# Kernel tuning notes

Hardware: AMD Instinct MI355X
Metric: run time of the kernel (lower is better)

Reference implementation:

```python
import jax, jax.numpy as jnp
import numpy as np

N = 100000   # num nodes
E = 1000000  # num edges
IN, H, OUT = 128, 64, 64
THR = 0.1      # lcs_threshold
LN_EPS = 1e-5


def setup_inputs() -> dict:
    key = jax.random.key(0)
    ks = jax.random.split(key, 8)
    x = jax.random.normal(ks[0], (N, IN), dtype=jnp.float32)
    edge_index = jax.random.randint(ks[1], (2, E), 0, N, dtype=jnp.int32)
    W1 = jax.random.normal(ks[2], (IN, H), dtype=jnp.float32) / np.float32(np.sqrt(IN))
    b1 = jnp.zeros((H,), jnp.float32)
    W2 = jax.random.normal(ks[3], (H, OUT), dtype=jnp.float32) / np.float32(np.sqrt(H))
    b2 = jnp.zeros((OUT,), jnp.float32)
    ln_gamma = jnp.ones((H,), jnp.float32)
    ln_beta = jnp.zeros((H,), jnp.float32)
    return {"x": x, "W1": W1, "b1": b1, "W2": W2, "b2": b2,
            "ln_gamma": ln_gamma, "ln_beta": ln_beta, "edge_index": edge_index}


def _gcn_conv(h_in, W, b, src, dst, ew, n):
    """PyG GCNConv: D^-1/2 (A+I) D^-1/2 (h_in @ W) + b, with edge weights ew.
    Masked edges (ew=0) contribute neither messages nor degree -> equivalent to
    filtering them out."""
    h = h_in @ W                                   # [n, d_out]
    deg = jax.ops.segment_sum(ew, dst, num_segments=n) + 1.0  # +1 self-loop
    dis = jax.lax.rsqrt(deg)                       # deg >= 1, finite
    norm = dis[src] * dis[dst] * ew                # [E]
    agg = jax.ops.segment_sum(h[src] * norm[:, None], dst, num_segments=n)
    agg = agg + h * (dis * dis)[:, None]           # self-loop term
    return agg + b


def _layer_norm(h, gamma, beta):
    mu = jnp.mean(h, axis=-1, keepdims=True)
    var = jnp.mean(jnp.square(h - mu), axis=-1, keepdims=True)
    return (h - mu) * jax.lax.rsqrt(var + LN_EPS) * gamma + beta


def reference(x, W1, b1, W2, b2, ln_gamma, ln_beta, edge_index):
    src, dst = edge_index[0], edge_index[1]
    n = x.shape[0]
    ones_e = jnp.ones((src.shape[0],), x.dtype)

    # layer 0: no LCS filtering (i == 0)
    h = _gcn_conv(x, W1, b1, src, dst, ones_e, n)
    h = _layer_norm(h, ln_gamma, ln_beta)
    h = jax.nn.relu(h)  # dropout: inference mode (identity)

    # layer 1: LCS filtering via node scores = min-max normalized L2 norm
    s = jnp.linalg.norm(h, axis=1)
    s = (s - s.min()) / (s.max() - s.min() + 1e-8)
    mask = (s[dst] > THR).astype(x.dtype)

    out = _gcn_conv(h, W2, b2, src, dst, mask, n)
    return jax.nn.log_softmax(out, axis=1)
```

## Files before the change

### kernel.cpp

```cpp
#include <hip/hip_runtime.h>
#include <math.h>

#define N_NODES 100000
#define N_EDGES 1000000
#define IN_F 128
#define H_F 64
#define THRV 0.1f
#define LN_EPS 1e-5f
#define GRID_AGG 2048

#define BSHIFT 9
#define NB 196
#define BCAP 6144
#define EPB 2048
#define NPB ((N_EDGES + EPB - 1) / EPB)

static __device__ __forceinline__ float wave_sum(float x) {
  for (int o = 32; o > 0; o >>= 1) x += __shfl_xor(x, o, 64);
  return x;
}
static __device__ __forceinline__ float wave_max(float x) {
  for (int o = 32; o > 0; o >>= 1) x = fmaxf(x, __shfl_xor(x, o, 64));
  return x;
}
static __device__ __forceinline__ unsigned short f2bf(float f) {
  unsigned u = __float_as_uint(f);
  u = (u + 0x7FFFu + ((u >> 16) & 1u)) >> 16;
  return (unsigned short)u;
}
static __device__ __forceinline__ float bf2f(unsigned short b) {
  return __uint_as_float(((unsigned)b) << 16);
}


__global__ __launch_bounds__(256) void k_part(const int* __restrict__ src,
                                              const int* __restrict__ dst,
                                              int* __restrict__ bcnt,
                                              int* __restrict__ part) {
  __shared__ int h[NB];
  __shared__ int cur[NB];
  int t = threadIdx.x;
  for (int i = t; i < NB; i += 256) h[i] = 0;
  __syncthreads();
  int base = blockIdx.x * EPB;
  int d[8];
#pragma unroll
  for (int i = 0; i < 8; ++i) {
    int e = base + t + i * 256;
    d[i] = (e < N_EDGES) ? dst[e] : -1;
  }
#pragma unroll
  for (int i = 0; i < 8; ++i)
    if (d[i] >= 0) atomicAdd(&h[d[i] >> BSHIFT], 1);
  __syncthreads();
  for (int i = t; i < NB; i += 256) {
    int c = h[i];
    cur[i] = c ? atomicAdd(&bcnt[i], c) : 0;
  }
  __syncthreads();
#pragma unroll
  for (int i = 0; i < 8; ++i) {
    if (d[i] >= 0) {
      int e = base + t + i * 256;
      int b = d[i] >> BSHIFT;
      int pos = atomicAdd(&cur[b], 1);
      part[b * BCAP + pos] = src[e] | ((d[i] & 511) << 17);
    }
  }
}

__global__ __launch_bounds__(256) void k_build(
    const int* __restrict__ part, const int* __restrict__ bcnt,
    int* __restrict__ indeg, int* __restrict__ offs, float* __restrict__ dis1,
    int* __restrict__ csr_src) {
  __shared__ int cnt[512];
  __shared__ int slds[256];
  int b = blockIdx.x;
  int t = threadIdx.x;
  int beg = b * BCAP;
  int end = beg + bcnt[b];
  for (int i = t; i < 512; i += 256) cnt[i] = 0;
  __syncthreads();
  for (int i = beg + t; i < end; i += 256)
    atomicAdd(&cnt[(part[i] >> 17) & 511], 1);
  __syncthreads();
  int a0 = cnt[2 * t], a1 = cnt[2 * t + 1];
  int pairsum = a0 + a1;
  slds[t] = pairsum;
  __syncthreads();
  int val = pairsum;
  for (int o = 1; o < 256; o <<= 1) {
    int y = (t >= o) ? slds[t - o] : 0;
    __syncthreads();
    val += y;
    slds[t] = val;
    __syncthreads();
  }
  int ex = val - pairsum;
  int off0 = ex, off1 = ex + a0;
  cnt[2 * t] = off0;
  cnt[2 * t + 1] = off1;
  int node0 = (b << BSHIFT) + 2 * t;
  if (node0 < N_NODES) {
    indeg[node0] = a0;
    offs[node0] = beg + off0;
    dis1[node0] = rsqrtf((float)a0 + 1.f);
  }
  if (node0 + 1 < N_NODES) {
    indeg[node0 + 1] = a1;
    offs[node0 + 1] = beg + off1;
    dis1[node0 + 1] = rsqrtf((float)a1 + 1.f);
  }
  __syncthreads();
  for (int i = beg + t; i < end; i += 256) {
    int p = part[i];
    int loc = (p >> 17) & 511;
    int pos = atomicAdd(&cnt[loc], 1);
    csr_src[beg + pos] = p & 131071;
  }
}

template <int K, int SCALEMODE>
__global__ __launch_bounds__(256) void k_gemm(const float* __restrict__ X,
                                              const float* __restrict__ W,
                                              const float* __restrict__ scale,
                                              const int* __restrict__ smm_i,
                                              const int* __restrict__ indeg,
                                              void* __restrict__ Yv, int nrows) {
  __shared__ __align__(16) float Ws[K][64];
  int t = threadIdx.x;
  for (int idx = t; idx < K * 16; idx += 256)
    ((float4*)&Ws[0][0])[idx] = ((const float4*)W)[idx];
  __syncthreads();

  int lane = t & 63;
  int wid = t >> 6;
  int tx = lane & 15, ty = lane >> 4;
  int rbase = blockIdx.x * 64 + wid * 16 + ty * 4;
  int r[4];
#pragma unroll
  for (int i = 0; i < 4; ++i) {
    int g = rbase + i;
    r[i] = (g < nrows) ? g : (nrows - 1);
  }
  int c0 = tx * 4;
  float acc[4][4] = {};

#pragma unroll 2
  for (int k = 0; k < K; k += 4) {
    float xv[4][4], wv[4][4];
#pragma unroll
    for (int i = 0; i < 4; ++i)
      *(float4*)xv[i] = *(const float4*)(X + (size_t)r[i] * K + k);
#pragma unroll
    for (int j = 0; j < 4; ++j)
      *(float4*)wv[j] = *(const float4*)&Ws[k + j][c0];
#pragma unroll
    for (int i = 0; i < 4; ++i)
#pragma unroll
      for (int kk = 0; kk < 4; ++kk)
#pragma unroll
        for (int j = 0; j < 4; ++j)
          acc[i][j] = fmaf(xv[i][kk], wv[kk][j], acc[i][j]);
  }

  float smin = 0.f, inv = 0.f;
  if constexpr (SCALEMODE == 1) {
    smin = __int_as_float(smm_i[0]);
    float smax = __int_as_float(smm_i[1]);
    inv = 1.f / (smax - smin + 1e-8f);
  }
#pragma unroll
  for (int i = 0; i < 4; ++i) {
    int gr = rbase + i;
    if (gr < nrows) {
      float sc;
      if constexpr (SCALEMODE == 1) {
        float sn = (scale[gr] - smin) * inv;
        float dmask = (sn > THRV) ? (float)indeg[gr] : 0.f;
        sc = rsqrtf(dmask + 1.f);
      } else {
        sc = scale[gr];
      }
      if constexpr (SCALEMODE == 1) {
        ushort4 o;
        o.x = f2bf(acc[i][0] * sc);
        o.y = f2bf(acc[i][1] * sc);
        o.z = f2bf(acc[i][2] * sc);
        o.w = f2bf(acc[i][3] * sc);
        *(ushort4*)((unsigned short*)Yv + (size_t)gr * 64 + c0) = o;
      } else {
        float4 o;
        o.x = acc[i][0] * sc;
        o.y = acc[i][1] * sc;
        o.z = acc[i][2] * sc;
        o.w = acc[i][3] * sc;
        *(float4*)((float*)Yv + (size_t)gr * 64 + c0) = o;
      }
    }
  }
}

__global__ __launch_bounds__(256) void k_agg1(
    const float* __restrict__ h1p, const int* __restrict__ offs,
    const int* __restrict__ indeg, const int* __restrict__ csr_src,
    const float* __restrict__ dis1, const float* __restrict__ b1,
    const float* __restrict__ gamma, const float* __restrict__ beta,
    float* __restrict__ h, float* __restrict__ s, int* __restrict__ smm_i) {
  int lane = threadIdx.x & 63;
  int wid = blockIdx.x * 4 + (threadIdx.x >> 6);
  int nw = gridDim.x * 4;
  float bmin = __builtin_inff(), bmax = -__builtin_inff();
  float b1l = b1[lane], gl = gamma[lane], bl = beta[lane];
  for (int v = wid; v < N_NODES; v += nw) {
    int beg = offs[v];
    int deg = indeg[v];
    float disv = dis1[v];
    float acc = h1p[v * 64 + lane];
    for (int c = 0; c < deg; c += 64) {
      int m = deg - c;
      if (m > 64) m = 64;
      int ul = (lane < m) ? csr_src[beg + c + lane] : 0;
      int j = 0;
      for (; j + 8 <= m; j += 8) {
        int u0 = __shfl(ul, j + 0), u1 = __shfl(ul, j + 1);
        int u2 = __shfl(ul, j + 2), u3 = __shfl(ul, j + 3);
        int u4 = __shfl(ul, j + 4), u5 = __shfl(ul, j + 5);
        int u6 = __shfl(ul, j + 6), u7 = __shfl(ul, j + 7);
        float a0 = h1p[u0 * 64 + lane], a1 = h1p[u1 * 64 + lane];
        float a2 = h1p[u2 * 64 + lane], a3 = h1p[u3 * 64 + lane];
        float a4 = h1p[u4 * 64 + lane], a5 = h1p[u5 * 64 + lane];
        float a6 = h1p[u6 * 64 + lane], a7 = h1p[u7 * 64 + lane];
        acc += ((a0 + a1) + (a2 + a3)) + ((a4 + a5) + (a6 + a7));
      }
      for (; j < m; ++j) {
        int u = __shfl(ul, j);
        acc += h1p[u * 64 + lane];
      }
    }
    acc = disv * acc + b1l;
    float mu = wave_sum(acc) * (1.f / 64.f);
    float d = acc - mu;
    float var = wave_sum(d * d) * (1.f / 64.f);
    float hn = d * rsqrtf(var + LN_EPS) * gl + bl;
    hn = fmaxf(hn, 0.f);
    h[v * 64 + lane] = hn;
    float sv = sqrtf(wave_sum(hn * hn));
    if (lane == 0) s[v] = sv;
    bmin = fminf(bmin, sv);
    bmax = fmaxf(bmax, sv);
  }
  __shared__ float lmin[4], lmax[4];
  if ((threadIdx.x & 63) == 0) {
    lmin[threadIdx.x >> 6] = bmin;
    lmax[threadIdx.x >> 6] = bmax;
  }
  __syncthreads();
  if (threadIdx.x == 0) {
    float mn = fminf(fminf(lmin[0], lmin[1]), fminf(lmin[2], lmin[3]));
    float mx = fmaxf(fmaxf(lmax[0], lmax[1]), fmaxf(lmax[2], lmax[3]));
    atomicMin(&smm_i[0], __float_as_int(mn));
    atomicMax(&smm_i[1], __float_as_int(mx));
  }
}

__global__ __launch_bounds__(256) void k_agg2(
    const unsigned short* __restrict__ h2b, const int* __restrict__ offs,
    const int* __restrict__ indeg, const int* __restrict__ csr_src,
    const float* __restrict__ s, const int* __restrict__ smm_i,
    const float* __restrict__ b2, float* __restrict__ out) {
  int lane = threadIdx.x & 63;
  int wid = blockIdx.x * 4 + (threadIdx.x >> 6);
  int nw = gridDim.x * 4;
  float smin = __int_as_float(smm_i[0]);
  float smax = __int_as_float(smm_i[1]);
  float inv = 1.f / (smax - smin + 1e-8f);
  float b2l = b2[lane];
  for (int v = wid; v < N_NODES; v += nw) {
    int deg = indeg[v];
    float sn = (s[v] - smin) * inv;
    bool on = sn > THRV;
    float acc = bf2f(h2b[v * 64 + lane]);
    if (on) {
      int beg = offs[v];
      for (int c = 0; c < deg; c += 64) {
        int m = deg - c;
        if (m > 64) m = 64;
        int ul = (lane < m) ? csr_src[beg + c + lane] : 0;
        int j = 0;
        for (; j + 8 <= m; j += 8) {
          int u0 = __shfl(ul, j + 0), u1 = __shfl(ul, j + 1);
          int u2 = __shfl(ul, j + 2), u3 = __shfl(ul, j + 3);
          int u4 = __shfl(ul, j + 4), u5 = __shfl(ul, j + 5);
          int u6 = __shfl(ul, j + 6), u7 = __shfl(ul, j + 7);
          float a0 = bf2f(h2b[u0 * 64 + lane]), a1 = bf2f(h2b[u1 * 64 + lane]);
          float a2 = bf2f(h2b[u2 * 64 + lane]), a3 = bf2f(h2b[u3 * 64 + lane]);
          float a4 = bf2f(h2b[u4 * 64 + lane]), a5 = bf2f(h2b[u5 * 64 + lane]);
          float a6 = bf2f(h2b[u6 * 64 + lane]), a7 = bf2f(h2b[u7 * 64 + lane]);
          acc += ((a0 + a1) + (a2 + a3)) + ((a4 + a5) + (a6 + a7));
        }
        for (; j < m; ++j) {
          int u = __shfl(ul, j);
          acc += bf2f(h2b[u * 64 + lane]);
        }
      }
    }
    float disv = rsqrtf((on ? (float)deg : 0.f) + 1.f);
    acc = disv * acc + b2l;
    float m = wave_max(acc);
    float p = expf(acc - m);
    float sum = wave_sum(p);
    out[v * 64 + lane] = acc - m - logf(sum);
  }
}

extern "C" void kernel_launch(void* const* d_in, const int* in_sizes, int n_in,
                              void* d_out, int out_size, void* d_ws, size_t ws_size,
                              hipStream_t stream) {
  const float* x = (const float*)d_in[0];
  const float* W1 = (const float*)d_in[1];
  const float* b1 = (const float*)d_in[2];
  const float* W2 = (const float*)d_in[3];
  const float* b2 = (const float*)d_in[4];
  const float* gamma = (const float*)d_in[5];
  const float* beta = (const float*)d_in[6];
  const int* ei = (const int*)d_in[7];
  const int* src = ei;
  const int* dst = ei + N_EDGES;
  float* out = (float*)d_out;

  char* ws = (char*)d_ws;
  size_t off = 0;
  auto alloc = [&](size_t bytes) {
    void* p = ws + off;
    off += (bytes + 255) & ~(size_t)255;
    return p;
  };
  int* indeg = (int*)alloc(N_NODES * 4);
  int* offs = (int*)alloc(N_NODES * 4);
  int* bcnt = (int*)alloc(NB * 4);
  int* smm_i = (int*)alloc(256);
  int* csr_src = (int*)alloc((size_t)NB * BCAP * 4);
  float* s = (float*)alloc(N_NODES * 4);
  float* dis1 = (float*)alloc(N_NODES * 4);
  float* h1 = (float*)alloc((size_t)N_NODES * 64 * 4);
  float* h = (float*)alloc((size_t)N_NODES * 64 * 4);
  int* part = (int*)h1;
  unsigned short* h2b = (unsigned short*)h1;
  (void)ws_size;
  (void)n_in;
  (void)in_sizes;
  (void)out_size;

  hipMemsetAsync(bcnt, 0, NB * 4, stream);
  hipMemsetAsync(&smm_i[0], 0x7F, 4, stream);
  hipMemsetAsync(&smm_i[1], 0x00, 4, stream);
  k_part<<<NPB, 256, 0, stream>>>(src, dst, bcnt, part);
  k_build<<<NB, 256, 0, stream>>>(part, bcnt, indeg, offs, dis1, csr_src);
  int gemm_grid = (N_NODES + 63) / 64;
  k_gemm<IN_F, 0><<<gemm_grid, 256, 0, stream>>>(x, W1, dis1, nullptr, nullptr,
                                                 h1, N_NODES);
  k_agg1<<<GRID_AGG, 256, 0, stream>>>(h1, offs, indeg, csr_src, dis1, b1, gamma,
                                       beta, h, s, smm_i);
  k_gemm<H_F, 1><<<gemm_grid, 256, 0, stream>>>(h, W2, s, smm_i, indeg, h2b,
                                                N_NODES);
  k_agg2<<<GRID_AGG, 256, 0, stream>>>(h2b, offs, indeg, csr_src, s, smm_i, b2,
                                       out);
}
```

Before: 242.1 us.

## Compact CSR with bucket prefix scan and replace atomic min/max with two-pass reduction

Adds a single-block scan over bucket counts so the CSR source array is stored densely (E entries) rather than with fixed BCAP-sized bucket strides. It also replaces the global atomicMin/atomicMax on float-as-int with per-block partial min/max plus a one-block reduction kernel, which removes two memsets. The cost is two extra tiny kernel launches. Bias and LayerNorm parameters are now reloaded per node instead of being held in registers.

```diff
diff --git a/kernel.cpp b/kernel.cpp
--- a/kernel.cpp
+++ b/kernel.cpp
@@ -69,19 +69,39 @@
   }
 }
 
+__global__ void k_bscan(const int* __restrict__ bcnt, int* __restrict__ bbase) {
+  __shared__ int lds[256];
+  int t = threadIdx.x;
+  int v = (t < NB) ? bcnt[t] : 0;
+  lds[t] = v;
+  __syncthreads();
+  int val = v;
+  for (int o = 1; o < 256; o <<= 1) {
+    int y = (t >= o) ? lds[t - o] : 0;
+    __syncthreads();
+    val += y;
+    lds[t] = val;
+    __syncthreads();
+  }
+  if (t < NB) bbase[t] = val - v;
+  if (t == 255) bbase[NB] = val;
+}
+
 __global__ __launch_bounds__(256) void k_build(
     const int* __restrict__ part, const int* __restrict__ bcnt,
-    int* __restrict__ indeg, int* __restrict__ offs, float* __restrict__ dis1,
+    const int* __restrict__ bbase, int* __restrict__ indeg,
+    int* __restrict__ offs, float* __restrict__ dis1,
     int* __restrict__ csr_src) {
   __shared__ int cnt[512];
   __shared__ int slds[256];
   int b = blockIdx.x;
   int t = threadIdx.x;
-  int beg = b * BCAP;
-  int end = beg + bcnt[b];
+  int pbeg = b * BCAP;
+  int pend = pbeg + bcnt[b];
+  int obeg = bbase[b];
   for (int i = t; i < 512; i += 256) cnt[i] = 0;
   __syncthreads();
-  for (int i = beg + t; i < end; i += 256)
+  for (int i = pbeg + t; i < pend; i += 256)
     atomicAdd(&cnt[(part[i] >> 17) & 511], 1);
   __syncthreads();
   int a0 = cnt[2 * t], a1 = cnt[2 * t + 1];
@@ -103,20 +123,20 @@
   int node0 = (b << BSHIFT) + 2 * t;
   if (node0 < N_NODES) {
     indeg[node0] = a0;
-    offs[node0] = beg + off0;
+    offs[node0] = obeg + off0;
     dis1[node0] = rsqrtf((float)a0 + 1.f);
   }
   if (node0 + 1 < N_NODES) {
     indeg[node0 + 1] = a1;
-    offs[node0 + 1] = beg + off1;
+    offs[node0 + 1] = obeg + off1;
     dis1[node0 + 1] = rsqrtf((float)a1 + 1.f);
   }
   __syncthreads();
-  for (int i = beg + t; i < end; i += 256) {
+  for (int i = pbeg + t; i < pend; i += 256) {
     int p = part[i];
     int loc = (p >> 17) & 511;
     int pos = atomicAdd(&cnt[loc], 1);
-    csr_src[beg + pos] = p & 131071;
+    csr_src[obeg + pos] = p & 131071;
   }
 }
 
@@ -124,7 +144,7 @@
 __global__ __launch_bounds__(256) void k_gemm(const float* __restrict__ X,
                                               const float* __restrict__ W,
                                               const float* __restrict__ scale,
-                                              const int* __restrict__ smm_i,
+                                              const float* __restrict__ smm,
                                               const int* __restrict__ indeg,
                                               void* __restrict__ Yv, int nrows) {
   __shared__ __align__(16) float Ws[K][64];
@@ -166,23 +186,17 @@
 
   float smin = 0.f, inv = 0.f;
   if constexpr (SCALEMODE == 1) {
-    smin = __int_as_float(smm_i[0]);
-    float smax = __int_as_float(smm_i[1]);
-    inv = 1.f / (smax - smin + 1e-8f);
+    smin = smm[0];
+    inv = 1.f / (smm[1] - smin + 1e-8f);
   }
 #pragma unroll
   for (int i = 0; i < 4; ++i) {
     int gr = rbase + i;
     if (gr < nrows) {
-      float sc;
       if constexpr (SCALEMODE == 1) {
         float sn = (scale[gr] - smin) * inv;
         float dmask = (sn > THRV) ? (float)indeg[gr] : 0.f;
-        sc = rsqrtf(dmask + 1.f);
-      } else {
-        sc = scale[gr];
-      }
-      if constexpr (SCALEMODE == 1) {
+        float sc = rsqrtf(dmask + 1.f);
         ushort4 o;
         o.x = f2bf(acc[i][0] * sc);
         o.y = f2bf(acc[i][1] * sc);
@@ -190,6 +204,7 @@
         o.w = f2bf(acc[i][3] * sc);
         *(ushort4*)((unsigned short*)Yv + (size_t)gr * 64 + c0) = o;
       } else {
+        float sc = scale[gr];
         float4 o;
         o.x = acc[i][0] * sc;
         o.y = acc[i][1] * sc;
@@ -206,12 +221,11 @@
     const int* __restrict__ indeg, const int* __restrict__ csr_src,
     const float* __restrict__ dis1, const float* __restrict__ b1,
     const float* __restrict__ gamma, const float* __restrict__ beta,
-    float* __restrict__ h, float* __restrict__ s, int* __restrict__ smm_i) {
+    float* __restrict__ h, float* __restrict__ s, float* __restrict__ mmpart) {
   int lane = threadIdx.x & 63;
   int wid = blockIdx.x * 4 + (threadIdx.x >> 6);
   int nw = gridDim.x * 4;
   float bmin = __builtin_inff(), bmax = -__builtin_inff();
-  float b1l = b1[lane], gl = gamma[lane], bl = beta[lane];
   for (int v = wid; v < N_NODES; v += nw) {
     int beg = offs[v];
     int deg = indeg[v];
@@ -238,11 +252,11 @@
         acc += h1p[u * 64 + lane];
       }
     }
-    acc = disv * acc + b1l;
+    acc = disv * acc + b1[lane];
     float mu = wave_sum(acc) * (1.f / 64.f);
     float d = acc - mu;
     float var = wave_sum(d * d) * (1.f / 64.f);
-    float hn = d * rsqrtf(var + LN_EPS) * gl + bl;
+    float hn = d * rsqrtf(var + LN_EPS) * gamma[lane] + beta[lane];
     hn = fmaxf(hn, 0.f);
     h[v * 64 + lane] = hn;
     float sv = sqrtf(wave_sum(hn * hn));
@@ -257,25 +271,42 @@
   }
   __syncthreads();
   if (threadIdx.x == 0) {
-    float mn = fminf(fminf(lmin[0], lmin[1]), fminf(lmin[2], lmin[3]));
-    float mx = fmaxf(fmaxf(lmax[0], lmax[1]), fmaxf(lmax[2], lmax[3]));
-    atomicMin(&smm_i[0], __float_as_int(mn));
-    atomicMax(&smm_i[1], __float_as_int(mx));
+    mmpart[blockIdx.x * 2] = fminf(fminf(lmin[0], lmin[1]), fminf(lmin[2], lmin[3]));
+    mmpart[blockIdx.x * 2 + 1] = fmaxf(fmaxf(lmax[0], lmax[1]), fmaxf(lmax[2], lmax[3]));
+  }
+}
+
+__global__ void k_minmax2(const float* __restrict__ mmpart, float* __restrict__ smm,
+                          int nblk) {
+  int t = threadIdx.x;
+  float mn = __builtin_inff(), mx = -__builtin_inff();
+  for (int i = t; i < nblk; i += 256) {
+    mn = fminf(mn, mmpart[i * 2]);
+    mx = fmaxf(mx, mmpart[i * 2 + 1]);
+  }
+  for (int o = 32; o; o >>= 1) {
+    mn = fminf(mn, __shfl_xor(mn, o, 64));
+    mx = fmaxf(mx, __shfl_xor(mx, o, 64));
+  }
+  __shared__ float a[4], b[4];
+  if ((t & 63) == 0) { a[t >> 6] = mn; b[t >> 6] = mx; }
+  __syncthreads();
+  if (t == 0) {
+    smm[0] = fminf(fminf(a[0], a[1]), fminf(a[2], a[3]));
+    smm[1] = fmaxf(fmaxf(b[0], b[1]), fmaxf(b[2], b[3]));
   }
 }
 
 __global__ __launch_bounds__(256) void k_agg2(
     const unsigned short* __restrict__ h2b, const int* __restrict__ offs,
     const int* __restrict__ indeg, const int* __restrict__ csr_src,
-    const float* __restrict__ s, const int* __restrict__ smm_i,
+    const float* __restrict__ s, const float* __restrict__ smm,
     const float* __restrict__ b2, float* __restrict__ out) {
   int lane = threadIdx.x & 63;
   int wid = blockIdx.x * 4 + (threadIdx.x >> 6);
   int nw = gridDim.x * 4;
-  float smin = __int_as_float(smm_i[0]);
-  float smax = __int_as_float(smm_i[1]);
-  float inv = 1.f / (smax - smin + 1e-8f);
-  float b2l = b2[lane];
+  float smin = smm[0];
+  float inv = 1.f / (smm[1] - smin + 1e-8f);
   for (int v = wid; v < N_NODES; v += nw) {
     int deg = indeg[v];
     float sn = (s[v] - smin) * inv;
@@ -306,7 +337,7 @@
       }
     }
     float disv = rsqrtf((on ? (float)deg : 0.f) + 1.f);
-    acc = disv * acc + b2l;
+    acc = disv * acc + b2[lane];
     float m = wave_max(acc);
     float p = expf(acc - m);
     float sum = wave_sum(p);
@@ -339,8 +370,10 @@
   int* indeg = (int*)alloc(N_NODES * 4);
   int* offs = (int*)alloc(N_NODES * 4);
   int* bcnt = (int*)alloc(NB * 4);
-  int* smm_i = (int*)alloc(256);
-  int* csr_src = (int*)alloc((size_t)NB * BCAP * 4);
+  int* bbase = (int*)alloc((NB + 1) * 4);
+  float* mmpart = (float*)alloc(GRID_AGG * 2 * 4);
+  float* smm = (float*)alloc(256);
+  int* csr_src = (int*)alloc((size_t)N_EDGES * 4);
   float* s = (float*)alloc(N_NODES * 4);
   float* dis1 = (float*)alloc(N_NODES * 4);
   float* h1 = (float*)alloc((size_t)N_NODES * 64 * 4);
@@ -353,17 +386,17 @@
   (void)out_size;
 
   hipMemsetAsync(bcnt, 0, NB * 4, stream);
-  hipMemsetAsync(&smm_i[0], 0x7F, 4, stream);
-  hipMemsetAsync(&smm_i[1], 0x00, 4, stream);
   k_part<<<NPB, 256, 0, stream>>>(src, dst, bcnt, part);
-  k_build<<<NB, 256, 0, stream>>>(part, bcnt, indeg, offs, dis1, csr_src);
+  k_bscan<<<1, 256, 0, stream>>>(bcnt, bbase);
+  k_build<<<NB, 256, 0, stream>>>(part, bcnt, bbase, indeg, offs, dis1, csr_src);
   int gemm_grid = (N_NODES + 63) / 64;
   k_gemm<IN_F, 0><<<gemm_grid, 256, 0, stream>>>(x, W1, dis1, nullptr, nullptr,
                                                  h1, N_NODES);
   k_agg1<<<GRID_AGG, 256, 0, stream>>>(h1, offs, indeg, csr_src, dis1, b1, gamma,
-                                       beta, h, s, smm_i);
-  k_gemm<H_F, 1><<<gemm_grid, 256, 0, stream>>>(h, W2, s, smm_i, indeg, h2b,
+                                       beta, h, s, mmpart);
+  k_minmax2<<<1, 256, 0, stream>>>(mmpart, smm, GRID_AGG);
+  k_gemm<H_F, 1><<<gemm_grid, 256, 0, stream>>>(h, W2, s, smm, indeg, h2b,
                                                 N_NODES);
-  k_agg2<<<GRID_AGG, 256, 0, stream>>>(h2b, offs, indeg, csr_src, s, smm_i, b2,
+  k_agg2<<<GRID_AGG, 256, 0, stream>>>(h2b, offs, indeg, csr_src, s, smm, b2,
                                        out);
 }
```

After: 207.1 us. 1.17x faster.
